# Performance work log

Measured on AMD Instinct MI355X. Metric: run time of the kernel, lower is better.

Reference implementation:

```python
import jax, jax.numpy as jnp
import numpy as np

DEPTH = 10
LEAF = 2 ** DEPTH          # 1024 leaves
NODE_NUM = 2 * LEAF - 1    # 2047
N = NODE_NUM + 1           # 2048 nodes incl. global node 0
ATTN = 4
D = 128
B = 8
L = 2


def _trace_children(ni):
    terms = []
    s, e = ni << 1, (ni << 1) | 1
    while s <= NODE_NUM and e <= NODE_NUM:
        terms.extend(range(s, e + 1))
        s <<= 1
        e = (e << 1) | 1
    return terms


def _trace_left(si):
    ni, cd, terms, stop = si + LEAF, DEPTH, [], False
    while not stop:
        cs = ni - ATTN + 1 - ((ni - ATTN + 1) & 1)
        stop = cs < 2 ** cd
        cs = max(2 ** cd, cs)
        terms.extend(range(cs, ni + 1))
        ni = (cs - 1) >> 1
        cd -= 1
    return terms


def _trace_right(ei):
    ni, cd, terms, stop = ei + LEAF, DEPTH, [], False
    while not stop:
        ce = ni + ATTN - 1 + ((ni - ATTN) & 1)
        stop = ce >= 2 ** (cd + 1)
        ce = min(2 ** (cd + 1) - 1, ce)
        terms.extend(range(ni, ce + 1))
        ni = (ce + 1) >> 1
        cd -= 1
    return terms


def _build_edges():
    src, dst = [], []
    for ni in range(1, NODE_NUM + 1):
        if ni < LEAF:
            t = _trace_children(ni)
        else:
            t = _trace_left(ni - LEAF) + _trace_right(ni - LEAF)
        src.extend(t)
        dst.extend([ni] * len(t))
    e = np.stack([np.asarray(src, np.int64), np.asarray(dst, np.int64)])  # [2, E]
    off = np.arange(B, dtype=np.int64) * N
    eb = (e[:, None, :] + off[None, :, None]).reshape(2, -1)  # batch-offset like _fetch_edge_data
    return eb.astype(np.int32)


def setup_inputs() -> dict:
    key = jax.random.key(0)
    k0, k1, k2 = jax.random.split(key, 3)
    s = 1.0 / np.sqrt(D)
    return {
        "elements": jax.random.normal(k0, (B, LEAF, D), jnp.float32),
        "ln_gamma": jnp.ones((L, D), jnp.float32),
        "ln_beta": jnp.zeros((L, D), jnp.float32),
        "w_nei": (jax.random.normal(k1, (L, D, D), jnp.float32) * s),
        "b_nei": jnp.zeros((L, D), jnp.float32),
        "w_root": (jax.random.normal(k2, (L, D, D), jnp.float32) * s),
        "edge_index": jnp.asarray(_build_edges()),
    }


def _sinusoid(pos, d):
    # ArbitraryPositionEncoder: sinusoidal encoding over (possibly negative) positions
    half = d // 2
    inv = jnp.exp(-jnp.arange(half, dtype=jnp.float32) * (np.log(10000.0) / half))
    ang = pos[:, None] * inv[None, :]  # [n, half]
    return jnp.stack([jnp.sin(ang), jnp.cos(ang)], -1).reshape(pos.shape[0], d)


def reference(elements, ln_gamma, ln_beta, w_nei, b_nei, w_root, edge_index):
    Bx, leaf, d = elements.shape
    depth = int(np.log2(leaf))
    # bottom-up tree compression (mean of two children)
    cur = elements
    levels = [cur]
    for _ in range(depth):
        cur = 0.5 * (cur[:, 0::2] + cur[:, 1::2])
        levels.append(cur)
    # node ordering: [global node 0 (=-1), root (level 0), ..., leaves (level depth)]
    node_feat = jnp.concatenate(
        [jnp.full((Bx, 1, d), -1.0, elements.dtype)] + levels[::-1], axis=1)  # [B, N, D]
    n = node_feat.shape[1]
    # positional encoding: vertical = floor(log2(idx)), horizontal = idx - 2^vertical
    idx = jnp.arange(n, dtype=jnp.float32)
    vpos = jnp.floor(jnp.log2(jnp.where(idx == 0, 0.5, idx)))
    hpos = idx - jnp.exp2(vpos)
    enc = jnp.concatenate([_sinusoid(hpos, d // 2), _sinusoid(vpos, d // 2)], -1)  # [N, D]
    x = (node_feat + enc[None]).reshape(Bx * n, d)
    src, dst = edge_index[0], edge_index[1]
    nseg = Bx * n
    deg = jnp.maximum(
        jax.ops.segment_sum(jnp.ones(src.shape, jnp.float32), dst, num_segments=nseg), 1.0)
    # DeepGCNLayer res+ blocks with SAGEConv (mean aggr)
    for l in range(ln_gamma.shape[0]):
        mu = jnp.mean(x, -1, keepdims=True)
        var = jnp.mean((x - mu) ** 2, -1, keepdims=True)
        h = (x - mu) * jax.lax.rsqrt(var + 1e-5) * ln_gamma[l] + ln_beta[l]
        h = jax.nn.gelu(h, approximate=False)
        agg = jax.ops.segment_sum(h[src], dst, num_segments=nseg) / deg[:, None]
        h = agg @ w_nei[l] + b_nei[l] + h @ w_root[l]
        x = x + h
    return x.reshape(Bx, n, d)
```

## Files before the change

kernel.cpp:

```cpp
#include <hip/hip_runtime.h>
#include <hip/hip_bf16.h>

#define LEAFN 1024
#define NN    2048
#define BATCH 8
#define DD    128
#define ROWS  (BATCH*NN)
#define AHS   384
#define NB    256
#define NT    1024

#define LOG1E4_OVER_32 0.28782313662425575f

#define SLACK 9
#define CSTRIDE 136
#define AGGL_OFF 54672
#define RED_OFF  63376

typedef __bf16 bf16x8 __attribute__((ext_vector_type(8)));
typedef float  floatx4 __attribute__((ext_vector_type(4)));
typedef float  floatx2 __attribute__((ext_vector_type(2)));

__device__ __forceinline__ float bf2f(unsigned short u) {
  return __uint_as_float(((unsigned)u) << 16);
}
__device__ __forceinline__ unsigned short f2bf(float f) {
  unsigned u = __float_as_uint(f);
  u += 0x7FFFu + ((u >> 16) & 1u);
  return (unsigned short)(u >> 16);
}
__device__ __forceinline__ float gelu(float v) {
  return 0.5f * v * (1.0f + erff(v * 0.70710678118f));
}
__device__ __forceinline__ floatx2 bfpair(unsigned u) {
  floatx2 r;
  r[0] = __uint_as_float(u << 16);
  r[1] = __uint_as_float(u & 0xffff0000u);
  return r;
}

__device__ __forceinline__ float enc_val(int node, int d) {
  float hp, vp;
  if (node == 0) { hp = -0.5f; vp = -1.0f; }
  else {
    int v = 31 - __clz(node);
    hp = (float)(node - (1 << v));
    vp = (float)v;
  }
  float pos = (d < 64) ? hp : vp;
  int i = ((d < 64) ? d : (d - 64)) >> 1;
  float inv = __expf(-(float)i * LOG1E4_OVER_32);
  float ang = pos * inv;
  return (d & 1) ? __cosf(ang) : __sinf(ang);
}

__device__ __forceinline__ void win_cd(int jb, int cd, int& lo_, int& wd_) {
  int g0 = 1024 + jb * 32, g1 = g0 + 31;
  int a0 = g0 >> (10 - cd), a1 = g1 >> (10 - cd);
  int l = a0 - SLACK, h = a1 + SLACK;
  int lvlo = 1 << cd, lvhi = (2 << cd) - 1;
  lo_ = l < lvlo ? lvlo : l;
  int hh = h > lvhi ? lvhi : h;
  int w = hh - lo_ + 1;
  wd_ = w < 0 ? 0 : w;
}

__device__ __forceinline__ void gbarN(int* bar, int slot) {
  __syncthreads();
  if (threadIdx.x == 0) {
    int g = blockIdx.x & 7;
    int* base = bar + (slot * 8 + g) * 64;
    __threadfence();
    if (__hip_atomic_fetch_add(base, 1, __ATOMIC_RELAXED,
                               __HIP_MEMORY_SCOPE_AGENT) == 31)
      __hip_atomic_store(base + 32, 1, __ATOMIC_RELAXED,
                         __HIP_MEMORY_SCOPE_AGENT);
    while (!__hip_atomic_load(base + 32, __ATOMIC_RELAXED,
                              __HIP_MEMORY_SCOPE_AGENT))
      __builtin_amdgcn_s_sleep(1);
    __threadfence();
  }
  __syncthreads();
}

__device__ __forceinline__ void ph_tree(char* smemc, int b, int s,
                                        const float* __restrict__ elements,
                                        float* __restrict__ x,
                                        float* __restrict__ lvl4,
                                        unsigned short* __restrict__ ah,
                                        const float* __restrict__ gamma,
                                        const float* __restrict__ beta,
                                        float* __restrict__ sroot,
                                        float* xci, int* bar) {
  float* sm = (float*)smemc;
  int tid = threadIdx.x;
  const float4* src = (const float4*)(elements + (size_t)(b * LEAFN + s * 64) * DD);
  for (int i = tid; i < 2048; i += NT) {
    int f = i * 4;
    int j = f >> 7, d = f & 127;
    *(float4*)&sm[(63 + j) * DD + d] = src[i];
  }
  __syncthreads();
  for (int lv = 5; lv >= 0; --lv) {
    int nodes = 1 << lv;
    for (int idx = tid; idx < nodes * DD; idx += NT) {
      int k = nodes + (idx >> 7);
      int d = idx & 127;
      sm[(k - 1) * DD + d] = 0.5f * (sm[(2 * k - 1) * DD + d] + sm[(2 * k) * DD + d]);
    }
    __syncthreads();
  }
  if (tid < DD) lvl4[(b * 16 + s) * DD + tid] = sm[tid];
  __syncthreads();
  if (tid == 0) {
    __threadfence();
    __hip_atomic_store(bar + 1536 + b * 64 + s * 4, 1, __ATOMIC_RELAXED,
                       __HIP_MEMORY_SCOPE_AGENT);
  }
  for (int idx = tid; idx < 127 * DD; idx += NT) {
    int k = (idx >> 7) + 1;
    int d = idx & 127;
    int lv = 31 - __clz(k);
    int g = ((16 + s) << lv) | (k - (1 << lv));
    float xv = sm[idx] + enc_val(g, d);
    if (k >= 64) x[((size_t)(b * NN + g)) * DD + d] = xv;
    sm[idx] = xv;
  }
  __syncthreads();
  {
    int wave = tid >> 6, lane = tid & 63;
    if (wave < 8) {
      int mt = wave >> 2, nq = wave & 3;
      int m = lane & 15, q = lane >> 4;
#pragma unroll
      for (int c = 0; c < 2; ++c)
#pragma unroll
        for (int ci = 0; ci < 2; ++ci)
#pragma unroll
          for (int r = 0; r < 4; ++r) {
            int t = c * 32 + mt * 16 + q * 4 + r;
            int k = (t == 63) ? 1 : t + 1;
            int d = (nq * 2 + ci) * 16 + m;
            xci[c * 8 + ci * 4 + r] = sm[(k - 1) * DD + d];
          }
    }
  }
  __syncthreads();
  {
    int sub = tid & 7, dp = sub * 16;
    for (int rr = tid >> 3; rr < 127; rr += NT / 8) {
      float* rowp = &sm[rr * DD + dp];
      float4 q0 = *(float4*)rowp;
      float4 q1 = *(float4*)(rowp + 4);
      float4 q2 = *(float4*)(rowp + 8);
      float4 q3 = *(float4*)(rowp + 12);
      float v[16] = {q0.x, q0.y, q0.z, q0.w, q1.x, q1.y, q1.z, q1.w,
                     q2.x, q2.y, q2.z, q2.w, q3.x, q3.y, q3.z, q3.w};
      float s1 = 0.f, s2 = 0.f;
#pragma unroll
      for (int j = 0; j < 16; ++j) { s1 += v[j]; s2 += v[j] * v[j]; }
      s1 += __shfl_xor(s1, 1); s2 += __shfl_xor(s2, 1);
      s1 += __shfl_xor(s1, 2); s2 += __shfl_xor(s2, 2);
      s1 += __shfl_xor(s1, 4); s2 += __shfl_xor(s2, 4);
      float mu = s1 * (1.0f / 128.0f);
      float var = s2 * (1.0f / 128.0f) - mu * mu;
      float rinv = rsqrtf(var + 1e-5f);
      int k = rr + 1, lv = 31 - __clz(k);
      int g = ((16 + s) << lv) | (k - (1 << lv));
      __attribute__((aligned(16))) unsigned short o[16];
      float hv[16];
#pragma unroll
      for (int j = 0; j < 16; ++j) {
        hv[j] = gelu((v[j] - mu) * rinv * gamma[dp + j] + beta[dp + j]);
        o[j] = f2bf(hv[j]);
      }
      *(float4*)rowp        = make_float4(hv[0], hv[1], hv[2], hv[3]);
      *(float4*)(rowp + 4)  = make_float4(hv[4], hv[5], hv[6], hv[7]);
      *(float4*)(rowp + 8)  = make_float4(hv[8], hv[9], hv[10], hv[11]);
      *(float4*)(rowp + 12) = make_float4(hv[12], hv[13], hv[14], hv[15]);
      unsigned short* dst = &ah[(size_t)(b * NN + g) * AHS + 128 + dp];
      *(uint4*)&dst[0] = *(uint4*)&o[0];
      *(uint4*)&dst[8] = *(uint4*)&o[8];
    }
  }
  __syncthreads();
  for (int lv = 5; lv >= 0; --lv) {
    int nk = 1 << lv;
    float inv = 1.0f / (float)((1 << (7 - lv)) - 2);
    for (int idx = tid; idx < nk * DD; idx += NT) {
      int k = nk + (idx >> 7);
      int d = idx & 127;
      float S = sm[(2 * k - 1) * DD + d] + sm[(2 * k) * DD + d];
      if (lv < 5) S += sm[(4 * k - 1) * DD + d] + sm[(4 * k + 1) * DD + d];
      sm[(2 * k - 1) * DD + d] = S;
      int g = ((16 + s) << lv) | (k - nk);
      ah[(size_t)(b * NN + g) * AHS + d] = f2bf(S * inv);
    }
    __syncthreads();
  }
  if (tid < DD) sroot[(size_t)(b * 16 + s) * DD + tid] = sm[DD + tid];
}

__device__ __forceinline__ void ph_top(char* smemc, int b,
                                       const float* __restrict__ lvl4,
                                       unsigned short* __restrict__ ah,
                                       const float* __restrict__ gamma,
                                       const float* __restrict__ beta) {
  float (*xs)[DD] = (float(*)[DD])smemc;
  int tid = threadIdx.x;
  if (tid < 128) {
    int d = tid;
    float v[16];
    for (int j = 0; j < 16; ++j) v[j] = lvl4[(b * 16 + j) * DD + d];
    for (int j = 0; j < 8; ++j) v[j] = 0.5f * (v[2 * j] + v[2 * j + 1]);
    for (int j = 0; j < 8; ++j) xs[8 + j][d] = v[j] + enc_val(8 + j, d);
    for (int j = 0; j < 4; ++j) v[j] = 0.5f * (v[2 * j] + v[2 * j + 1]);
    for (int j = 0; j < 4; ++j) xs[4 + j][d] = v[j] + enc_val(4 + j, d);
    for (int j = 0; j < 2; ++j) v[j] = 0.5f * (v[2 * j] + v[2 * j + 1]);
    for (int j = 0; j < 2; ++j) xs[2 + j][d] = v[j] + enc_val(2 + j, d);
    v[0] = 0.5f * (v[0] + v[1]);
    xs[1][d] = v[0] + enc_val(1, d);
    xs[0][d] = -1.0f + enc_val(0, d);
  }
  __syncthreads();
  if (tid < 128) {
    int rr = tid >> 3, sub = tid & 7, dp = sub * 16;
    float w[16], s1 = 0.f, s2 = 0.f;
#pragma unroll
    for (int j = 0; j < 16; ++j) { w[j] = xs[rr][dp + j]; s1 += w[j]; s2 += w[j] * w[j]; }
    s1 += __shfl_xor(s1, 1); s2 += __shfl_xor(s2, 1);
    s1 += __shfl_xor(s1, 2); s2 += __shfl_xor(s2, 2);
    s1 += __shfl_xor(s1, 4); s2 += __shfl_xor(s2, 4);
    float mu = s1 * (1.0f / 128.0f);
    float var = s2 * (1.0f / 128.0f) - mu * mu;
    float rinv = rsqrtf(var + 1e-5f);
    __attribute__((aligned(16))) unsigned short o[16];
#pragma unroll
    for (int j = 0; j < 16; ++j)
      o[j] = f2bf(gelu((w[j] - mu) * rinv * gamma[dp + j] + beta[dp + j]));
    unsigned short* dst = &ah[(size_t)(b * NN + rr) * AHS + 128 + dp];
    *(uint4*)&dst[0] = *(uint4*)&o[0];
    *(uint4*)&dst[8] = *(uint4*)&o[8];
  }
  __syncthreads();
}

__device__ __forceinline__ void ph_aggsub(char* smemc, int b, int s,
                                          unsigned short* ah,
                                          float* __restrict__ sroot) {
  floatx4 (*S)[32] = (floatx4(*)[32])smemc;
  int tid = threadIdx.x;
  for (int idx = tid; idx < 32 * 32; idx += NT) {
    int k = 32 + (idx >> 5), q = idx & 31;
    int c = (16 + s) * 64 + (2 * k - 64);
    size_t a0 = (size_t)(b * NN + c) * AHS + 256 + q * 4;
    ushort4 u0 = *(const ushort4*)&ah[a0];
    ushort4 u1 = *(const ushort4*)&ah[a0 + AHS];
    floatx4 v;
    v[0] = bf2f(u0.x) + bf2f(u1.x);
    v[1] = bf2f(u0.y) + bf2f(u1.y);
    v[2] = bf2f(u0.z) + bf2f(u1.z);
    v[3] = bf2f(u0.w) + bf2f(u1.w);
    S[k][q] = v;
    int g = (16 + s) * 32 + (k - 32);
    int r = b * NN + g;
    ushort4 o;
    o.x = f2bf(v[0] * 0.5f); o.y = f2bf(v[1] * 0.5f);
    o.z = f2bf(v[2] * 0.5f); o.w = f2bf(v[3] * 0.5f);
    *(ushort4*)&ah[(size_t)r * AHS + q * 4] = o;
  }
  __syncthreads();
  for (int lv = 4; lv >= 0; --lv) {
    int nk = 1 << lv;
    float inv = 1.0f / (float)((1 << (7 - lv)) - 2);
    for (int idx = tid; idx < nk * 32; idx += NT) {
      int k = nk + (idx >> 5), q = idx & 31;
      int c = ((16 + s) << (lv + 1)) | (2 * k - 2 * nk);
      size_t a0 = (size_t)(b * NN + c) * AHS + 256 + q * 4;
      ushort4 u0 = *(const ushort4*)&ah[a0];
      ushort4 u1 = *(const ushort4*)&ah[a0 + AHS];
      floatx4 sc0 = S[2 * k][q], sc1 = S[2 * k + 1][q];
      floatx4 v;
      v[0] = bf2f(u0.x) + bf2f(u1.x) + sc0[0] + sc1[0];
      v[1] = bf2f(u0.y) + bf2f(u1.y) + sc0[1] + sc1[1];
      v[2] = bf2f(u0.z) + bf2f(u1.z) + sc0[2] + sc1[2];
      v[3] = bf2f(u0.w) + bf2f(u1.w) + sc0[3] + sc1[3];
      S[k][q] = v;
      int g = ((16 + s) << lv) | (k - nk);
      int r = b * NN + g;
      ushort4 o;
      o.x = f2bf(v[0] * inv); o.y = f2bf(v[1] * inv);
      o.z = f2bf(v[2] * inv); o.w = f2bf(v[3] * inv);
      *(ushort4*)&ah[(size_t)r * AHS + q * 4] = o;
    }
    __syncthreads();
  }
  for (int q = tid; q < 32; q += NT)
    ((floatx4*)sroot)[(size_t)(b * 16 + s) * 32 + q] = S[1][q];
}

__device__ __forceinline__ void ph_leafagg(char* smemc, int b, int jb,
                                           const int* __restrict__ srcv,
                                           const int* __restrict__ s0a,
                                           const int* __restrict__ s1a,
                                           const unsigned short* __restrict__ eoff,
                                           unsigned short* ah, int hoff) {
  unsigned short* cache = (unsigned short*)smemc;
  int tid = threadIdx.x;
  int lo[11], wd[11], off[11];
  int acc_off = 0;
#pragma unroll
  for (int cd = 10; cd >= 1; --cd) {
    win_cd(jb, cd, lo[cd], wd[cd]);
    off[cd] = acc_off;
    acc_off += wd[cd];
  }
#pragma unroll
  for (int cd = 10; cd >= 1; --cd) {
    int w = wd[cd];
    for (int t = tid; t < w * 16; t += NT) {
      int row = t >> 4, seg = t & 15;
      *(uint4*)&cache[(off[cd] + row) * CSTRIDE + seg * 8] =
          *(const uint4*)&ah[(size_t)(b * NN + lo[cd] + row) * AHS + hoff + seg * 8];
    }
  }
  __syncthreads();

  int leaf = tid >> 5, half = (tid >> 4) & 1, c = tid & 15;
  int r = b * NN + 1024 + jb * 32 + leaf;
  int e0 = s0a[r], e1 = s1a[r];
  int n = e1 - e0;
  int mid = e0 + (n >> 1);
  int ebeg = half ? mid : e0;
  int eend = half ? e1 : mid;
  int cb = c * 16;
  floatx2 a0 = {0.f, 0.f}, a1 = {0.f, 0.f}, a2 = {0.f, 0.f}, a3 = {0.f, 0.f};
  auto one = [&](int ei) {
    unsigned o = eoff[ei];
    uint4 u;
    if (o != 0xFFFFu)
      u = *(const uint4*)(smemc + o + cb);
    else {
      int g = srcv[ei] - b * NN;
      u = *(const uint4*)&ah[(size_t)(b * NN + g) * AHS + hoff + c * 8];
    }
    a0 += bfpair(u.x); a1 += bfpair(u.y); a2 += bfpair(u.z); a3 += bfpair(u.w);
  };
  int e = ebeg;
  for (; e + 4 <= eend; e += 4) {
    unsigned o0 = eoff[e], o1 = eoff[e + 1], o2 = eoff[e + 2], o3 = eoff[e + 3];
    if (!((((o0 + 1) | (o1 + 1) | (o2 + 1) | (o3 + 1)) >> 16))) {
      uint4 u0 = *(const uint4*)(smemc + o0 + cb);
      uint4 u1 = *(const uint4*)(smemc + o1 + cb);
      uint4 u2 = *(const uint4*)(smemc + o2 + cb);
      uint4 u3 = *(const uint4*)(smemc + o3 + cb);
      a0 += bfpair(u0.x); a1 += bfpair(u0.y); a2 += bfpair(u0.z); a3 += bfpair(u0.w);
      a0 += bfpair(u1.x); a1 += bfpair(u1.y); a2 += bfpair(u1.z); a3 += bfpair(u1.w);
      a0 += bfpair(u2.x); a1 += bfpair(u2.y); a2 += bfpair(u2.z); a3 += bfpair(u2.w);
      a0 += bfpair(u3.x); a1 += bfpair(u3.y); a2 += bfpair(u3.z); a3 += bfpair(u3.w);
    } else {
      one(e); one(e + 1); one(e + 2); one(e + 3);
    }
  }
  for (; e < eend; ++e) one(e);
  a0[0] += __shfl_xor(a0[0], 16); a0[1] += __shfl_xor(a0[1], 16);
  a1[0] += __shfl_xor(a1[0], 16); a1[1] += __shfl_xor(a1[1], 16);
  a2[0] += __shfl_xor(a2[0], 16); a2[1] += __shfl_xor(a2[1], 16);
  a3[0] += __shfl_xor(a3[0], 16); a3[1] += __shfl_xor(a3[1], 16);
  if (!half) {
    float inv = 1.0f / (float)max(n, 1);
    unsigned short* aggl = (unsigned short*)(smemc + AGGL_OFF);
    __attribute__((aligned(16))) unsigned short o[8];
    o[0] = f2bf(a0[0] * inv); o[1] = f2bf(a0[1] * inv);
    o[2] = f2bf(a1[0] * inv); o[3] = f2bf(a1[1] * inv);
    o[4] = f2bf(a2[0] * inv); o[5] = f2bf(a2[1] * inv);
    o[6] = f2bf(a3[0] * inv); o[7] = f2bf(a3[1] * inv);
    *(uint4*)&aggl[leaf * CSTRIDE + c * 8] = *(uint4*)&o[0];
  }
}

__device__ __forceinline__ void ph_topfin(int b,
                                          const float* __restrict__ sroot,
                                          unsigned short* ah, int hoff) {
  int d = threadIdx.x;
  float S16[16], h16[16], Sv[16];
#pragma unroll
  for (int j = 0; j < 16; ++j) S16[j] = sroot[(size_t)(b * 16 + j) * DD + d];
#pragma unroll
  for (int j = 0; j < 16; ++j)
    h16[j] = bf2f(ah[(size_t)(b * NN + 16 + j) * AHS + hoff + d]);
#pragma unroll
  for (int k = 8; k < 16; ++k)
    Sv[k] = h16[2 * k - 16] + h16[2 * k - 15] + S16[2 * k - 16] + S16[2 * k - 15];
#pragma unroll
  for (int k = 7; k >= 1; --k)
    Sv[k] = bf2f(ah[(size_t)(b * NN + 2 * k) * AHS + hoff + d]) +
            bf2f(ah[(size_t)(b * NN + 2 * k + 1) * AHS + hoff + d]) +
            Sv[2 * k] + Sv[2 * k + 1];
#pragma unroll
  for (int k = 1; k < 16; ++k) {
    int dv = 31 - __clz(k);
    float inv = 1.0f / (float)((1 << (11 - dv)) - 2);
    ah[(size_t)(b * NN + k) * AHS + d] = f2bf(Sv[k] * inv);
  }
  ah[(size_t)(b * NN) * AHS + d] = f2bf(0.0f);
}

__device__ __forceinline__ void ph_gemm32(char* redc, const unsigned short* aggl,
                                          int rowbase, unsigned short* ah,
                                          const unsigned short* __restrict__ wfl,
                                          const float* __restrict__ bn,
                                          float* __restrict__ x, int hoff_in,
                                          const float* __restrict__ gamma,
                                          const float* __restrict__ beta,
                                          float* xc, int first_layer) {
  int wave = threadIdx.x >> 6, lane = threadIdx.x & 63;
  bool act = wave < 8;
  int mt = (wave & 7) >> 2, nq = wave & 3;
  int r0 = rowbase + mt * 16;
  int m = lane & 15, q = lane >> 4;
  floatx4 acc[2];
  acc[0] = (floatx4){0.f, 0.f, 0.f, 0.f};
  acc[1] = (floatx4){0.f, 0.f, 0.f, 0.f};
  if (act) {
    const unsigned short* arow = ah + (size_t)(r0 + m) * AHS + q * 8;
    const bf16x8* B = (const bf16x8*)wfl + lane;
#pragma unroll
    for (int kc = 0; kc < 8; ++kc) {
      bf16x8 a0;
      if (kc < 4)
        a0 = *(const bf16x8*)&aggl[(mt * 16 + m) * CSTRIDE + kc * 32 + q * 8];
      else
        a0 = *(const bf16x8*)(arow + hoff_in + (kc - 4) * 32);
#pragma unroll
      for (int ci = 0; ci < 2; ++ci) {
        bf16x8 bb = B[(kc * 8 + nq * 2 + ci) * 64];
        acc[ci] = __builtin_amdgcn_mfma_f32_16x16x32_bf16(a0, bb, acc[ci], 0, 0, 0);
      }
    }
  }
  if (first_layer) {
    float s1[4] = {0.f, 0.f, 0.f, 0.f}, s2[4] = {0.f, 0.f, 0.f, 0.f};
    if (act) {
#pragma unroll
      for (int ci = 0; ci < 2; ++ci) {
        int col = (nq * 2 + ci) * 16 + m;
        float bias = bn[col];
#pragma unroll
        for (int r = 0; r < 4; ++r) {
          int row = r0 + q * 4 + r;
          float v = x[(size_t)row * DD + col] + acc[ci][r] + bias;
          xc[ci * 4 + r] = v;
          s1[r] += v; s2[r] += v * v;
        }
      }
#pragma unroll
      for (int r = 0; r < 4; ++r) {
        s1[r] += __shfl_xor(s1[r], 1); s2[r] += __shfl_xor(s2[r], 1);
        s1[r] += __shfl_xor(s1[r], 2); s2[r] += __shfl_xor(s2[r], 2);
        s1[r] += __shfl_xor(s1[r], 4); s2[r] += __shfl_xor(s2[r], 4);
        s1[r] += __shfl_xor(s1[r], 8); s2[r] += __shfl_xor(s2[r], 8);
      }
    }
    float* red = (float*)redc;
    int rl = mt * 16 + q * 4;
    __syncthreads();
    if (act && m == 0) {
#pragma unroll
      for (int r = 0; r < 4; ++r) {
        red[(rl + r) * 4 + nq] = s1[r];
        red[128 + (rl + r) * 4 + nq] = s2[r];
      }
    }
    __syncthreads();
    if (act) {
      float mu[4], rv[4];
#pragma unroll
      for (int r = 0; r < 4; ++r) {
        float t1 = red[(rl + r) * 4] + red[(rl + r) * 4 + 1] +
                   red[(rl + r) * 4 + 2] + red[(rl + r) * 4 + 3];
        float t2 = red[128 + (rl + r) * 4] + red[128 + (rl + r) * 4 + 1] +
                   red[128 + (rl + r) * 4 + 2] + red[128 + (rl + r) * 4 + 3];
        mu[r] = t1 * (1.0f / 128.0f);
        float var = t2 * (1.0f / 128.0f) - mu[r] * mu[r];
        rv[r] = rsqrtf(var + 1e-5f);
      }
#pragma unroll
      for (int ci = 0; ci < 2; ++ci) {
        int col = (nq * 2 + ci) * 16 + m;
        float gm = gamma[col], bt = beta[col];
#pragma unroll
        for (int r = 0; r < 4; ++r) {
          int row = r0 + q * 4 + r;
          float hh = gelu((xc[ci * 4 + r] - mu[r]) * rv[r] * gm + bt);
          ah[(size_t)row * AHS + 256 + col] = f2bf(hh);
        }
      }
    }
  } else {
    if (act) {
#pragma unroll
      for (int ci = 0; ci < 2; ++ci) {
        int col = (nq * 2 + ci) * 16 + m;
        float bias = bn[col];
#pragma unroll
        for (int r = 0; r < 4; ++r) {
          int row = r0 + q * 4 + r;
          x[(size_t)row * DD + col] = xc[ci * 4 + r] + acc[ci][r] + bias;
        }
      }
    }
  }
}

__device__ __forceinline__ void ph_gemm32s(char* redc, int b, int sb, int tbase,
                                           unsigned short* ah,
                                           const unsigned short* __restrict__ wfl,
                                           const float* __restrict__ bn,
                                           float* __restrict__ x, int hoff_in,
                                           const float* __restrict__ gamma,
                                           const float* __restrict__ beta,
                                           float* xc, int first_layer) {
  int wave = threadIdx.x >> 6, lane = threadIdx.x & 63;
  bool act = wave < 8;
  int mt = (wave & 7) >> 2, nq = wave & 3;
  int m = lane & 15, q = lane >> 4;
  int tA = tbase + mt * 16 + m;
  int kA = (tA == 63) ? 1 : tA + 1;
  int lvA = 31 - __clz(kA);
  int rowA = b * NN + (((16 + sb) << lvA) | (kA - (1 << lvA)));
  int rowO[4];
#pragma unroll
  for (int r = 0; r < 4; ++r) {
    int t = tbase + mt * 16 + q * 4 + r;
    int k = (t == 63) ? 1 : t + 1;
    int lv = 31 - __clz(k);
    rowO[r] = b * NN + (((16 + sb) << lv) | (k - (1 << lv)));
  }
  floatx4 acc[2];
  acc[0] = (floatx4){0.f, 0.f, 0.f, 0.f};
  acc[1] = (floatx4){0.f, 0.f, 0.f, 0.f};
  if (act) {
    const unsigned short* arow = ah + (size_t)rowA * AHS + q * 8;
    const bf16x8* B = (const bf16x8*)wfl + lane;
#pragma unroll
    for (int kc = 0; kc < 8; ++kc) {
      int koff = (kc < 4) ? kc * 32 : hoff_in + (kc - 4) * 32;
      bf16x8 a0 = *(const bf16x8*)(arow + koff);
#pragma unroll
      for (int ci = 0; ci < 2; ++ci) {
        bf16x8 bb = B[(kc * 8 + nq * 2 + ci) * 64];
        acc[ci] = __builtin_amdgcn_mfma_f32_16x16x32_bf16(a0, bb, acc[ci], 0, 0, 0);
      }
    }
  }
  if (first_layer) {
    float s1[4] = {0.f, 0.f, 0.f, 0.f}, s2[4] = {0.f, 0.f, 0.f, 0.f};
    if (act) {
#pragma unroll
      for (int ci = 0; ci < 2; ++ci) {
        int col = (nq * 2 + ci) * 16 + m;
        float bias = bn[col];
#pragma unroll
        for (int r = 0; r < 4; ++r) {
          float v = xc[ci * 4 + r] + acc[ci][r] + bias;
          xc[ci * 4 + r] = v;
          s1[r] += v; s2[r] += v * v;
        }
      }
#pragma unroll
      for (int r = 0; r < 4; ++r) {
        s1[r] += __shfl_xor(s1[r], 1); s2[r] += __shfl_xor(s2[r], 1);
        s1[r] += __shfl_xor(s1[r], 2); s2[r] += __shfl_xor(s2[r], 2);
        s1[r] += __shfl_xor(s1[r], 4); s2[r] += __shfl_xor(s2[r], 4);
        s1[r] += __shfl_xor(s1[r], 8); s2[r] += __shfl_xor(s2[r], 8);
      }
    }
    float* red = (float*)redc;
    int rl = mt * 16 + q * 4;
    __syncthreads();
    if (act && m == 0) {
#pragma unroll
      for (int r = 0; r < 4; ++r) {
        red[(rl + r) * 4 + nq] = s1[r];
        red[128 + (rl + r) * 4 + nq] = s2[r];
      }
    }
    __syncthreads();
    if (act) {
      float mu[4], rv[4];
#pragma unroll
      for (int r = 0; r < 4; ++r) {
        float t1 = red[(rl + r) * 4] + red[(rl + r) * 4 + 1] +
                   red[(rl + r) * 4 + 2] + red[(rl + r) * 4 + 3];
        float t2 = red[128 + (rl + r) * 4] + red[128 + (rl + r) * 4 + 1] +
                   red[128 + (rl + r) * 4 + 2] + red[128 + (rl + r) * 4 + 3];
        mu[r] = t1 * (1.0f / 128.0f);
        float var = t2 * (1.0f / 128.0f) - mu[r] * mu[r];
        rv[r] = rsqrtf(var + 1e-5f);
      }
#pragma unroll
      for (int ci = 0; ci < 2; ++ci) {
        int col = (nq * 2 + ci) * 16 + m;
        float gm = gamma[col], bt = beta[col];
#pragma unroll
        for (int r = 0; r < 4; ++r) {
          float hh = gelu((xc[ci * 4 + r] - mu[r]) * rv[r] * gm + bt);
          ah[(size_t)rowO[r] * AHS + 256 + col] = f2bf(hh);
        }
      }
    }
  } else {
    if (act) {
#pragma unroll
      for (int ci = 0; ci < 2; ++ci) {
        int col = (nq * 2 + ci) * 16 + m;
        float bias = bn[col];
#pragma unroll
        for (int r = 0; r < 4; ++r)
          x[(size_t)rowO[r] * DD + col] = xc[ci * 4 + r] + acc[ci][r] + bias;
      }
    }
  }
}

__device__ __forceinline__ void ph_gemm16t(char* redc, int b,
                                           unsigned short* ah,
                                           const unsigned short* __restrict__ wfl,
                                           const float* __restrict__ bn,
                                           float* __restrict__ x, int hoff_in,
                                           const float* __restrict__ gamma,
                                           const float* __restrict__ beta,
                                           float* xc, int first_layer) {
  int ct = threadIdx.x >> 6, lane = threadIdx.x & 63;
  bool act = ct < 8;
  int m = lane & 15, q = lane >> 4;
  floatx4 acc = (floatx4){0.f, 0.f, 0.f, 0.f};
  int col = (ct & 7) * 16 + m;
  if (act) {
    const unsigned short* arow = ah + (size_t)(b * NN + m) * AHS + q * 8;
    const bf16x8* B = (const bf16x8*)wfl + lane;
#pragma unroll
    for (int kc = 0; kc < 8; ++kc) {
      int koff = (kc < 4) ? kc * 32 : hoff_in + (kc - 4) * 32;
      bf16x8 a0 = *(const bf16x8*)(arow + koff);
      bf16x8 bb = B[(kc * 8 + ct) * 64];
      acc = __builtin_amdgcn_mfma_f32_16x16x32_bf16(a0, bb, acc, 0, 0, 0);
    }
  }
  if (first_layer) {
    float s1[4] = {0.f, 0.f, 0.f, 0.f}, s2[4] = {0.f, 0.f, 0.f, 0.f};
    float bias = act ? bn[col] : 0.f;
    if (act) {
#pragma unroll
      for (int r = 0; r < 4; ++r) {
        float v = xc[r] + acc[r] + bias;
        xc[r] = v; s1[r] = v; s2[r] = v * v;
      }
#pragma unroll
      for (int r = 0; r < 4; ++r) {
        s1[r] += __shfl_xor(s1[r], 1); s2[r] += __shfl_xor(s2[r], 1);
        s1[r] += __shfl_xor(s1[r], 2); s2[r] += __shfl_xor(s2[r], 2);
        s1[r] += __shfl_xor(s1[r], 4); s2[r] += __shfl_xor(s2[r], 4);
        s1[r] += __shfl_xor(s1[r], 8); s2[r] += __shfl_xor(s2[r], 8);
      }
    }
    float* red = (float*)redc;
    __syncthreads();
    if (act && m == 0) {
#pragma unroll
      for (int r = 0; r < 4; ++r) {
        red[(q * 4 + r) * 8 + ct] = s1[r];
        red[128 + (q * 4 + r) * 8 + ct] = s2[r];
      }
    }
    __syncthreads();
    if (act) {
#pragma unroll
      for (int r = 0; r < 4; ++r) {
        float t1 = 0.f, t2 = 0.f;
#pragma unroll
        for (int j = 0; j < 8; ++j) {
          t1 += red[(q * 4 + r) * 8 + j];
          t2 += red[128 + (q * 4 + r) * 8 + j];
        }
        float mu = t1 * (1.0f / 128.0f);
        float var = t2 * (1.0f / 128.0f) - mu * mu;
        float rv = rsqrtf(var + 1e-5f);
        float hh = gelu((xc[r] - mu) * rv * gamma[col] + beta[col]);
        ah[(size_t)(b * NN + q * 4 + r) * AHS + 256 + col] = f2bf(hh);
      }
    }
  } else {
    if (act) {
      float bias = bn[col];
#pragma unroll
      for (int r = 0; r < 4; ++r)
        x[(size_t)(b * NN + q * 4 + r) * DD + col] = xc[r] + acc[r] + bias;
    }
  }
}

__global__ __launch_bounds__(NT, 1) void k_mega(
    const float* __restrict__ elements, const float* __restrict__ ln_gamma,
    const float* __restrict__ ln_beta, const float* __restrict__ w_nei,
    const float* __restrict__ b_nei, const float* __restrict__ w_root,
    const int* __restrict__ srcv, const int* __restrict__ dstv, int E,
    float* __restrict__ x, int* s0a, int* s1a, float* lvl4, float* sroot,
    unsigned short* wf, unsigned short* ah, unsigned short* eoff, int* bar) {
  __shared__ __align__(16) char smem[65536];
  int bid = blockIdx.x, tid = threadIdx.x;
  int b = bid & 7, gb = bid >> 3;
  int Eb = E >> 3;
  unsigned short* wfg = wf + (size_t)b * 65536;
  float xcl[8], xci[16], xct[4];

  if (gb < 16) {
    ph_tree(smem, b, gb, elements, x, lvl4, ah, ln_gamma, ln_beta, sroot, xci, bar);
  } else if (gb < 24) {
    int base = b * Eb;
    for (int i = base + (gb - 16) * NT + tid; i < base + Eb; i += 8 * NT) {
      int dv = dstv[i];
      if (i == 0 || dstv[i - 1] != dv) s0a[dv] = i;
      if (i == base + Eb - 1 || dstv[i + 1] != dv) s1a[dv] = i + 1;
    }
    for (int i = base + (gb - 16) * NT + tid; i < base + Eb; i += 8 * NT) {
      int dl = dstv[i] - b * NN - 1024;
      unsigned short ov = 0xFFFFu;
      if (dl >= 0) {
        int jb2 = dl >> 5;
        int g = srcv[i] - b * NN;
        int lv = 31 - __clz(g);
        int acc2 = 0;
#pragma unroll
        for (int cd = 10; cd >= 1; --cd) {
          int lo_, wd_;
          win_cd(jb2, cd, lo_, wd_);
          if (cd == lv) {
            int idx = g - lo_;
            if ((unsigned)idx < (unsigned)wd_)
              ov = (unsigned short)((acc2 + idx) * (2 * CSTRIDE));
          }
          acc2 += wd_;
        }
      }
      eoff[i] = ov;
    }
    if (gb == 16) {
      if (tid < 16) {
        while (!__hip_atomic_load(bar + 1536 + b * 64 + tid * 4, __ATOMIC_RELAXED,
                                  __HIP_MEMORY_SCOPE_AGENT))
          __builtin_amdgcn_s_sleep(1);
        __threadfence();
      }
      __syncthreads();
      ph_top(smem, b, lvl4, ah, ln_gamma, ln_beta);
      {
        int wv = tid >> 6, ln = tid & 63, m_ = ln & 15, q_ = ln >> 4;
        if (wv < 8) {
          float (*xs)[DD] = (float(*)[DD])smem;
#pragma unroll
          for (int r = 0; r < 4; ++r) xct[r] = xs[q_ * 4 + r][wv * 16 + m_];
        }
      }
    }
  } else {
    int gi = (gb - 24) * NT + tid;
    if (gi < 4096) {
      int lane = gi & 63, ct = (gi >> 6) & 7, kc = gi >> 9;
      int n = ct * 16 + (lane & 15);
      int k = kc * 32 + (lane >> 4) * 8;
      int kk = k & 127;
#pragma unroll
      for (int l = 0; l < 2; ++l) {
        const float* w = (k < 128) ? (w_nei + (size_t)l * DD * DD)
                                   : (w_root + (size_t)l * DD * DD);
        unsigned short* o = wfg + (size_t)l * 32768 + (size_t)gi * 8;
#pragma unroll
        for (int j = 0; j < 8; ++j) o[j] = f2bf(w[(size_t)(kk + j) * DD + n]);
      }
    }
  }
  gbarN(bar, 0);

  if (gb == 16) {
    if (tid < 128) ph_topfin(b, sroot, ah, 128);
    __syncthreads();
    ph_gemm16t(smem + RED_OFF, b, ah, wfg, b_nei, x, 128,
               ln_gamma + DD, ln_beta + DD, xct, 1);
    __syncthreads();
  }
  ph_leafagg(smem, b, gb, srcv, s0a, s1a, eoff, ah, 128);
  __syncthreads();
  ph_gemm32(smem + RED_OFF, (const unsigned short*)(smem + AGGL_OFF),
            b * NN + 1024 + gb * 32, ah, wfg, b_nei, x, 128,
            ln_gamma + DD, ln_beta + DD, xcl, 1);
  if (gb < 16) {
    ph_gemm32s(smem + RED_OFF, b, gb, 0, ah, wfg, b_nei, x, 128,
               ln_gamma + DD, ln_beta + DD, xci, 1);
    ph_gemm32s(smem + RED_OFF, b, gb, 32, ah, wfg, b_nei, x, 128,
               ln_gamma + DD, ln_beta + DD, xci + 8, 1);
  }
  gbarN(bar, 1);

  if (gb < 16) {
    ph_aggsub(smem, b, gb, ah, sroot);
    __syncthreads();
    if (tid == 0) {
      __threadfence();
      __hip_atomic_store(bar + 1024 + b * 64 + gb * 4, 1, __ATOMIC_RELAXED,
                         __HIP_MEMORY_SCOPE_AGENT);
    }
  }
  ph_leafagg(smem, b, gb, srcv, s0a, s1a, eoff, ah, 256);
  __syncthreads();
  ph_gemm32(smem + RED_OFF, (const unsigned short*)(smem + AGGL_OFF),
            b * NN + 1024 + gb * 32, ah, wfg + 32768, b_nei + DD,
            x, 256, ln_gamma, ln_beta, xcl, 0);
  if (gb < 16) {
    ph_gemm32s(smem + RED_OFF, b, gb, 0, ah, wfg + 32768, b_nei + DD, x, 256,
               ln_gamma, ln_beta, xci, 0);
    ph_gemm32s(smem + RED_OFF, b, gb, 32, ah, wfg + 32768, b_nei + DD, x, 256,
               ln_gamma, ln_beta, xci + 8, 0);
  } else if (gb == 16) {
    if (tid < 16) {
      while (!__hip_atomic_load(bar + 1024 + b * 64 + tid * 4, __ATOMIC_RELAXED,
                                __HIP_MEMORY_SCOPE_AGENT))
        __builtin_amdgcn_s_sleep(1);
      __threadfence();
    }
    __syncthreads();
    if (tid < 128) ph_topfin(b, sroot, ah, 256);
    __syncthreads();
    ph_gemm16t(smem + RED_OFF, b, ah, wfg + 32768, b_nei + DD, x, 256,
               ln_gamma, ln_beta, xct, 0);
  }
}

extern "C" void kernel_launch(void* const* d_in, const int* in_sizes, int n_in,
                              void* d_out, int out_size, void* d_ws, size_t ws_size,
                              hipStream_t stream) {
  const float* elements = (const float*)d_in[0];
  const float* ln_gamma = (const float*)d_in[1];
  const float* ln_beta  = (const float*)d_in[2];
  const float* w_nei    = (const float*)d_in[3];
  const float* b_nei    = (const float*)d_in[4];
  const float* w_root   = (const float*)d_in[5];
  const int*   edge     = (const int*)d_in[6];
  int E = in_sizes[6] / 2;
  const int* srcv = edge;
  const int* dstv = edge + E;
  float* x = (float*)d_out;

  char* ws = (char*)d_ws;
  int*            bar   = (int*)ws;
  int*            s0    = (int*)(ws + 65536);
  int*            s1    = (int*)(ws + 131072);
  float*          lvl4  = (float*)(ws + 196608);
  float*          sroot = (float*)(ws + 262144);
  unsigned short* wf    = (unsigned short*)(ws + 327680);
  unsigned short* ah    = (unsigned short*)(ws + 327680 + 1048576);
  unsigned short* eoff  = (unsigned short*)(ws + 327680 + 1048576 + 12582912);

  hipMemsetAsync(bar, 0, 8192, stream);
  k_mega<<<dim3(NB), dim3(NT), 0, stream>>>(
      elements, ln_gamma, ln_beta, w_nei, b_nei, w_root,
      srcv, dstv, E, x, s0, s1, lvl4, sroot, wf, ah, eoff, bar);
}
```

Before: 169.0 us.

## Run internal-node GEMMs on idle upper waves and move top block to gb 28

The two internal-node GEMM tiles each block used to run serially after its leaf GEMM on waves 0-7 are now split. Waves 8-15, previously idle, run one internal tile concurrently with the leaf GEMM, using a separate reduction scratch area. Blocks 16-31 take over the other internal tile, reading their residual input from global x, which is now also written for nodes k<=32. The top-of-tree work moves from block 16 to block 28 to make room. This shortens the per-block critical path but adds extra global traffic and needs the launch grid to cover those extra blocks.

```diff
diff --git a/kernel.cpp b/kernel.cpp
--- a/kernel.cpp
+++ b/kernel.cpp
@@ -16,6 +16,7 @@
 #define CSTRIDE 136
 #define AGGL_OFF 54672
 #define RED_OFF  63376
+#define RED2_OFF 64400
 
 typedef __bf16 bf16x8 __attribute__((ext_vector_type(8)));
 typedef float  floatx4 __attribute__((ext_vector_type(4)));
@@ -123,26 +124,25 @@
     int lv = 31 - __clz(k);
     int g = ((16 + s) << lv) | (k - (1 << lv));
     float xv = sm[idx] + enc_val(g, d);
-    if (k >= 64) x[((size_t)(b * NN + g)) * DD + d] = xv;
+    if (k >= 64 || k <= 32) x[((size_t)(b * NN + g)) * DD + d] = xv;
     sm[idx] = xv;
   }
   __syncthreads();
   {
     int wave = tid >> 6, lane = tid & 63;
-    if (wave < 8) {
-      int mt = wave >> 2, nq = wave & 3;
+    if (wave >= 8) {
+      int wl = wave & 7;
+      int mt = wl >> 2, nq = wl & 3;
       int m = lane & 15, q = lane >> 4;
 #pragma unroll
-      for (int c = 0; c < 2; ++c)
-#pragma unroll
-        for (int ci = 0; ci < 2; ++ci)
-#pragma unroll
-          for (int r = 0; r < 4; ++r) {
-            int t = c * 32 + mt * 16 + q * 4 + r;
-            int k = (t == 63) ? 1 : t + 1;
-            int d = (nq * 2 + ci) * 16 + m;
-            xci[c * 8 + ci * 4 + r] = sm[(k - 1) * DD + d];
-          }
+      for (int ci = 0; ci < 2; ++ci)
+#pragma unroll
+        for (int r = 0; r < 4; ++r) {
+          int t = 32 + mt * 16 + q * 4 + r;
+          int k = (t == 63) ? 1 : t + 1;
+          int d = (nq * 2 + ci) * 16 + m;
+          xci[ci * 4 + r] = sm[(k - 1) * DD + d];
+        }
     }
   }
   __syncthreads();
@@ -416,7 +416,8 @@
                                           float* xc, int first_layer) {
   int wave = threadIdx.x >> 6, lane = threadIdx.x & 63;
   bool act = wave < 8;
-  int mt = (wave & 7) >> 2, nq = wave & 3;
+  int wl = wave & 7;
+  int mt = wl >> 2, nq = wl & 3;
   int r0 = rowbase + mt * 16;
   int m = lane & 15, q = lane >> 4;
   floatx4 acc[2];
@@ -520,10 +521,12 @@
                                            float* __restrict__ x, int hoff_in,
                                            const float* __restrict__ gamma,
                                            const float* __restrict__ beta,
-                                           float* xc, int first_layer) {
+                                           float* xc, int first_layer,
+                                           const float* __restrict__ gx) {
   int wave = threadIdx.x >> 6, lane = threadIdx.x & 63;
-  bool act = wave < 8;
-  int mt = (wave & 7) >> 2, nq = wave & 3;
+  bool act = wave >= 8;
+  int wl = wave & 7;
+  int mt = wl >> 2, nq = wl & 3;
   int m = lane & 15, q = lane >> 4;
   int tA = tbase + mt * 16 + m;
   int kA = (tA == 63) ? 1 : tA + 1;
@@ -563,7 +566,8 @@
         float bias = bn[col];
 #pragma unroll
         for (int r = 0; r < 4; ++r) {
-          float v = xc[ci * 4 + r] + acc[ci][r] + bias;
+          float x0 = gx ? gx[(size_t)rowO[r] * DD + col] : xc[ci * 4 + r];
+          float v = x0 + acc[ci][r] + bias;
           xc[ci * 4 + r] = v;
           s1[r] += v; s2[r] += v * v;
         }
@@ -713,7 +717,8 @@
   int b = bid & 7, gb = bid >> 3;
   int Eb = E >> 3;
   unsigned short* wfg = wf + (size_t)b * 65536;
-  float xcl[8], xci[16], xct[4];
+  float xcl[8], xci[8], xct[4];
+  int wv = tid >> 6;
 
   if (gb < 16) {
     ph_tree(smem, b, gb, elements, x, lvl4, ah, ln_gamma, ln_beta, sroot, xci, bar);
@@ -746,44 +751,41 @@
       }
       eoff[i] = ov;
     }
-    if (gb == 16) {
-      if (tid < 16) {
-        while (!__hip_atomic_load(bar + 1536 + b * 64 + tid * 4, __ATOMIC_RELAXED,
-                                  __HIP_MEMORY_SCOPE_AGENT))
-          __builtin_amdgcn_s_sleep(1);
-        __threadfence();
-      }
-      __syncthreads();
-      ph_top(smem, b, lvl4, ah, ln_gamma, ln_beta);
-      {
-        int wv = tid >> 6, ln = tid & 63, m_ = ln & 15, q_ = ln >> 4;
-        if (wv < 8) {
-          float (*xs)[DD] = (float(*)[DD])smem;
-#pragma unroll
-          for (int r = 0; r < 4; ++r) xct[r] = xs[q_ * 4 + r][wv * 16 + m_];
-        }
-      }
-    }
-  } else {
+  } else if (gb < 28) {
     int gi = (gb - 24) * NT + tid;
-    if (gi < 4096) {
-      int lane = gi & 63, ct = (gi >> 6) & 7, kc = gi >> 9;
-      int n = ct * 16 + (lane & 15);
-      int k = kc * 32 + (lane >> 4) * 8;
-      int kk = k & 127;
-#pragma unroll
-      for (int l = 0; l < 2; ++l) {
-        const float* w = (k < 128) ? (w_nei + (size_t)l * DD * DD)
-                                   : (w_root + (size_t)l * DD * DD);
-        unsigned short* o = wfg + (size_t)l * 32768 + (size_t)gi * 8;
-#pragma unroll
-        for (int j = 0; j < 8; ++j) o[j] = f2bf(w[(size_t)(kk + j) * DD + n]);
+    int lane = gi & 63, ct = (gi >> 6) & 7, kc = gi >> 9;
+    int n = ct * 16 + (lane & 15);
+    int k = kc * 32 + (lane >> 4) * 8;
+    int kk = k & 127;
+#pragma unroll
+    for (int l = 0; l < 2; ++l) {
+      const float* w = (k < 128) ? (w_nei + (size_t)l * DD * DD)
+                                 : (w_root + (size_t)l * DD * DD);
+      unsigned short* o = wfg + (size_t)l * 32768 + (size_t)gi * 8;
+#pragma unroll
+      for (int j = 0; j < 8; ++j) o[j] = f2bf(w[(size_t)(kk + j) * DD + n]);
+    }
+  } else if (gb == 28) {
+    if (tid < 16) {
+      while (!__hip_atomic_load(bar + 1536 + b * 64 + tid * 4, __ATOMIC_RELAXED,
+                                __HIP_MEMORY_SCOPE_AGENT))
+        __builtin_amdgcn_s_sleep(1);
+      __threadfence();
+    }
+    __syncthreads();
+    ph_top(smem, b, lvl4, ah, ln_gamma, ln_beta);
+    {
+      int ln = tid & 63, m_ = ln & 15, q_ = ln >> 4;
+      if (wv < 8) {
+        float (*xs)[DD] = (float(*)[DD])smem;
+#pragma unroll
+        for (int r = 0; r < 4; ++r) xct[r] = xs[q_ * 4 + r][wv * 16 + m_];
       }
     }
   }
   gbarN(bar, 0);
 
-  if (gb == 16) {
+  if (gb == 28) {
     if (tid < 128) ph_topfin(b, sroot, ah, 128);
     __syncthreads();
     ph_gemm16t(smem + RED_OFF, b, ah, wfg, b_nei, x, 128,
@@ -792,14 +794,16 @@
   }
   ph_leafagg(smem, b, gb, srcv, s0a, s1a, eoff, ah, 128);
   __syncthreads();
-  ph_gemm32(smem + RED_OFF, (const unsigned short*)(smem + AGGL_OFF),
-            b * NN + 1024 + gb * 32, ah, wfg, b_nei, x, 128,
-            ln_gamma + DD, ln_beta + DD, xcl, 1);
-  if (gb < 16) {
-    ph_gemm32s(smem + RED_OFF, b, gb, 0, ah, wfg, b_nei, x, 128,
-               ln_gamma + DD, ln_beta + DD, xci, 1);
-    ph_gemm32s(smem + RED_OFF, b, gb, 32, ah, wfg, b_nei, x, 128,
-               ln_gamma + DD, ln_beta + DD, xci + 8, 1);
+  if (wv < 8) {
+    ph_gemm32(smem + RED_OFF, (const unsigned short*)(smem + AGGL_OFF),
+              b * NN + 1024 + gb * 32, ah, wfg, b_nei, x, 128,
+              ln_gamma + DD, ln_beta + DD, xcl, 1);
+  } else if (gb < 16) {
+    ph_gemm32s(smem + RED2_OFF, b, gb, 32, ah, wfg, b_nei, x, 128,
+               ln_gamma + DD, ln_beta + DD, xci, 1, nullptr);
+  } else {
+    ph_gemm32s(smem + RED2_OFF, b, gb - 16, 0, ah, wfg, b_nei, x, 128,
+               ln_gamma + DD, ln_beta + DD, xci, 1, x);
   }
   gbarN(bar, 1);
 
@@ -814,15 +818,18 @@
   }
   ph_leafagg(smem, b, gb, srcv, s0a, s1a, eoff, ah, 256);
   __syncthreads();
-  ph_gemm32(smem + RED_OFF, (const unsigned short*)(smem + AGGL_OFF),
-            b * NN + 1024 + gb * 32, ah, wfg + 32768, b_nei + DD,
-            x, 256, ln_gamma, ln_beta, xcl, 0);
-  if (gb < 16) {
-    ph_gemm32s(smem + RED_OFF, b, gb, 0, ah, wfg + 32768, b_nei + DD, x, 256,
-               ln_gamma, ln_beta, xci, 0);
-    ph_gemm32s(smem + RED_OFF, b, gb, 32, ah, wfg + 32768, b_nei + DD, x, 256,
-               ln_gamma, ln_beta, xci + 8, 0);
-  } else if (gb == 16) {
+  if (wv < 8) {
+    ph_gemm32(smem + RED_OFF, (const unsigned short*)(smem + AGGL_OFF),
+              b * NN + 1024 + gb * 32, ah, wfg + 32768, b_nei + DD,
+              x, 256, ln_gamma, ln_beta, xcl, 0);
+  } else if (gb < 16) {
+    ph_gemm32s(smem + RED2_OFF, b, gb, 32, ah, wfg + 32768, b_nei + DD, x, 256,
+               ln_gamma, ln_beta, xci, 0, nullptr);
+  } else {
+    ph_gemm32s(smem + RED2_OFF, b, gb - 16, 0, ah, wfg + 32768, b_nei + DD, x, 256,
+               ln_gamma, ln_beta, xci, 0, nullptr);
+  }
+  if (gb == 28) {
     if (tid < 16) {
       while (!__hip_atomic_load(bar + 1024 + b * 64 + tid * 4, __ATOMIC_RELAXED,
                                 __HIP_MEMORY_SCOPE_AGENT))
```

Result: faster. 161.7 us (-4.3%).
